# Kernel tuning notes

Measured on AMD Instinct MI355X. Metric: run time of the kernel, lower is better.

Reference implementation:

```python
import jax, jax.numpy as jnp
import numpy as np

# SpargeAttn / spas_sage2_attn_meansim block sizes
BLKQ, BLKK = 128, 64
NUM_HEADS = 8
SIMTHRESHD1 = 0.6
CDFTHRESHD = 0.98


def _block_meta(t, blk):
    # t: [B,H,S,D] -> block means [B,H,nb,D] and min-cosine-to-mean per block [B,H,nb]
    B, H, S, D = t.shape
    nb = S // blk
    tb = t.reshape(B, H, nb, blk, D)
    m = tb.mean(axis=3)
    tn = tb / (jnp.linalg.norm(tb, axis=-1, keepdims=True) + 1e-6)
    mn = m / (jnp.linalg.norm(m, axis=-1, keepdims=True) + 1e-6)
    cos = jnp.einsum('bhnkd,bhnd->bhnk', tn, mn)
    return m, cos.min(axis=-1)


def _meansim_sparse_attention(q, k, v, scale):
    # Block-sparse attention with mean-similarity pruning (SpargeAttn meansim).
    qm, qsim = _block_meta(q, BLKQ)          # [B,H,nq,D], [B,H,nq]
    km, ksim = _block_meta(k, BLKK)          # [B,H,nk,D], [B,H,nk]
    q_self = qsim > SIMTHRESHD1              # self-similar Q blocks -> mean is representative
    k_self = ksim > SIMTHRESHD1
    # pooled attention map over block means
    pooled = jax.nn.softmax(jnp.einsum('bhqd,bhkd->bhqk', qm, km) * scale, axis=-1)
    # per Q-block row: keep highest-prob K blocks until cumulative mass >= cdfthreshd
    order = jnp.argsort(-pooled, axis=-1)
    sp = jnp.take_along_axis(pooled, order, axis=-1)
    csum = jnp.cumsum(sp, axis=-1)
    keep_sorted = (csum - sp) < CDFTHRESHD   # always keeps at least the top block
    inv = jnp.argsort(order, axis=-1)
    keep = jnp.take_along_axis(keep_sorted, inv, axis=-1)  # [B,H,nq,nk]
    # conservative fallback: non-self-similar Q/K blocks are never pruned
    block_mask = keep | (~q_self)[..., None] | (~k_self)[:, :, None, :]
    tok_mask = jnp.repeat(jnp.repeat(block_mask, BLKQ, axis=2), BLKK, axis=3)
    s = jnp.einsum('bhqd,bhkd->bhqk', q, k) * scale
    s = jnp.where(tok_mask, s, -jnp.inf)
    p = jax.nn.softmax(s, axis=-1)
    return jnp.einsum('bhqk,bhkd->bhqd', p, v)


def setup_inputs() -> dict:
    key = jax.random.key(0)
    B, L, C = 2, 2048, 512
    ks = jax.random.split(key, 3)
    x = jax.random.normal(ks[0], (B, L, C), jnp.float32)
    Wqkv = jax.random.normal(ks[1], (C, 3 * C), jnp.float32) * (C ** -0.5)
    bqkv = jnp.zeros((3 * C,), jnp.float32)
    Wproj = jax.random.normal(ks[2], (C, C), jnp.float32) * (C ** -0.5)
    bproj = jnp.zeros((C,), jnp.float32)
    return {"x": x, "Wqkv": Wqkv, "bqkv": bqkv, "Wproj": Wproj, "bproj": bproj}


def reference(x, Wqkv, bqkv, Wproj, bproj):
    B, L, C = x.shape
    H = NUM_HEADS
    D = C // H
    scale = D ** -0.5
    qkv = (x @ Wqkv + bqkv).reshape(B, L, 3, H, D)
    qkv = jnp.transpose(qkv, (2, 0, 3, 1, 4))  # [3,B,H,L,D]
    q, k, v = qkv[0], qkv[1], qkv[2]
    o = _meansim_sparse_attention(q, k, v, scale)  # [B,H,L,D]
    o = jnp.transpose(o, (0, 2, 1, 3)).reshape(B, L, C)
    return o @ Wproj + bproj
```

## Files before the change

### kernel.cpp

```cpp
#include <hip/hip_runtime.h>
#include <math.h>

typedef unsigned short ushortT;
typedef unsigned int uintT;
typedef __attribute__((ext_vector_type(8))) short short8;
typedef __attribute__((ext_vector_type(16))) float f32x16;
#define MFMA32(a, b, c) __builtin_amdgcn_mfma_f32_32x32x16_bf16((a), (b), (c), 0, 0, 0)


#define LOG2E 1.4426950408889634f

static __device__ __forceinline__ ushortT f2b(float f) {
    union { float f; uintT u; } v; v.f = f;
    uintT u = v.u;
    u += 0x7fffu + ((u >> 16) & 1u);
    return (ushortT)(u >> 16);
}
static __device__ __forceinline__ uintT pack2(float a, float b) {
    return (uintT)f2b(a) | ((uintT)f2b(b) << 16);
}
static __device__ __forceinline__ uintT pack2t(float a, float b) {
    union { float f; uintT u; } x0, x1; x0.f = a; x1.f = b;
    return __builtin_amdgcn_perm(x1.u, x0.u, 0x07060302u);
}
static __device__ __forceinline__ float blo(uintT u) {
    union { uintT u; float f; } v; v.u = u << 16; return v.f;
}
static __device__ __forceinline__ float bhi(uintT u) {
    union { uintT u; float f; } v; v.u = u & 0xffff0000u; return v.f;
}
static __device__ __forceinline__ f32x16 zero16() {
    f32x16 z;
    #pragma unroll
    for (int i = 0; i < 16; ++i) z[i] = 0.f;
    return z;
}

#define NQB 16
#define NKB 32

__global__ __launch_bounds__(256) void prep_kernel(
    const float* __restrict__ x, ushortT* __restrict__ xb,
    const float* __restrict__ Wq, ushortT* __restrict__ Wqt,
    const float* __restrict__ Wp, ushortT* __restrict__ Wpt) {
    const int bid = blockIdx.x, t = threadIdx.x;
    __shared__ float tile[32][33];
    if (bid < 2048) {
        int i = (bid * 256 + t) * 4;
        float4 v = *(const float4*)(x + i);
        uint2 o; o.x = pack2(v.x, v.y); o.y = pack2(v.z, v.w);
        *(uint2*)(xb + i) = o;
        return;
    }
    const float* W; ushortT* Wt; int C, c0, r0;
    if (bid < 2816) {
        const int b = bid - 2048;
        W = Wq; Wt = Wqt; C = 1536;
        c0 = (b % 48) * 32; r0 = (b / 48) * 32;
    } else {
        const int b = bid - 2816;
        W = Wp; Wt = Wpt; C = 512;
        c0 = (b & 15) * 32; r0 = (b >> 4) * 32;
    }
    const int tx = t & 31, ty = t >> 5;
    #pragma unroll
    for (int i = 0; i < 4; ++i)
        tile[ty + 8 * i][tx] = W[(size_t)(r0 + ty + 8 * i) * C + c0 + tx];
    __syncthreads();
    #pragma unroll
    for (int i = 0; i < 4; ++i) {
        int rr = ty + 8 * i;
        Wt[(size_t)(c0 + rr) * 512 + r0 + tx] = f2b(tile[tx][rr]);
    }
}

__global__ __launch_bounds__(256) void qkv_gemm_kernel(
    const ushortT* __restrict__ xb, const ushortT* __restrict__ wt,
    const float* __restrict__ bias,
    ushortT* __restrict__ qb, ushortT* __restrict__ kbuf, ushortT* __restrict__ vt,
    float* __restrict__ qm, float* __restrict__ km,
    float* __restrict__ qs, float* __restrict__ ks) {
    __shared__ __align__(16) ushortT As[2][128 * 40];
    __shared__ __align__(16) ushortT Bs[2][64 * 40];
    __shared__ float sumbuf[4][64];
    __shared__ float meanS[2][64];
    __shared__ float wminS[4];
    const int t = threadIdx.x;
    const int l = t & 63, w = t >> 6;
    const int lm = l & 31, lh = l >> 5;
    const int rowbase = blockIdx.y * 128;
    const int colbase = blockIdx.x * 64;

    f32x16 acc[2];
    acc[0] = zero16(); acc[1] = zero16();

    const int r = t >> 1, half = t & 1;
    const ushortT* Ag = xb + (size_t)(rowbase + r) * 512 + half * 16;
    const int soA = r * 40 + half * 16;
    const int rb = t >> 2, q4 = t & 3;
    const ushortT* Bg = wt + (size_t)(colbase + rb) * 512 + q4 * 8;
    const int soB = rb * 40 + q4 * 8;

    uint4 a0, a1, b0;
    a0 = *(const uint4*)(Ag); a1 = *(const uint4*)(Ag + 8);
    b0 = *(const uint4*)(Bg);
    *(uint4*)(&As[0][soA]) = a0; *(uint4*)(&As[0][soA] + 8) = a1;
    *(uint4*)(&Bs[0][soB]) = b0;

    for (int k0 = 0; k0 < 512; k0 += 32) {
        const int cur = (k0 >> 5) & 1;
        __syncthreads();
        if (k0 < 480) {
            a0 = *(const uint4*)(Ag + k0 + 32); a1 = *(const uint4*)(Ag + k0 + 40);
            b0 = *(const uint4*)(Bg + k0 + 32);
        }
        #pragma unroll
        for (int ks2 = 0; ks2 < 2; ++ks2) {
            const int ko = 16 * ks2 + 8 * lh;
            short8 af  = *(const short8*)(&As[cur][(32 * w + lm) * 40 + ko]);
            short8 b_0 = *(const short8*)(&Bs[cur][lm * 40 + ko]);
            short8 b_1 = *(const short8*)(&Bs[cur][(32 + lm) * 40 + ko]);
            acc[0] = MFMA32(af, b_0, acc[0]);
            acc[1] = MFMA32(af, b_1, acc[1]);
        }
        if (k0 < 480) {
            const int nxt = cur ^ 1;
            *(uint4*)(&As[nxt][soA]) = a0; *(uint4*)(&As[nxt][soA] + 8) = a1;
            *(uint4*)(&Bs[nxt][soB]) = b0;
        }
    }

    const int which = blockIdx.x >> 3;
    const int h = blockIdx.x & 7;
    const int by = blockIdx.y;
    const int b = by >> 4;
    const size_t hb = (size_t)(b * 8 + h);
    float bias2[2];
    #pragma unroll
    for (int nt = 0; nt < 2; ++nt) bias2[nt] = bias[colbase + 32 * nt + lm];
    float msum[2] = {0.f, 0.f};
    #pragma unroll
    for (int nt = 0; nt < 2; ++nt) {
        const int dd = 32 * nt + lm;
        #pragma unroll
        for (int rg = 0; rg < 16; ++rg) {
            const int row_local = 32 * w + (rg & 3) + 8 * (rg >> 2) + 4 * lh;
            const int ll = (rowbase + row_local) & 2047;
            float val = acc[nt][rg] + bias2[nt];
            if (which == 0) {
                val *= 0.125f;
                msum[nt] += val;
                qb[(hb * 2048 + ll) * 64 + dd] = f2b(val * LOG2E);
            } else if (which == 1) {
                msum[nt] += val;
                kbuf[(hb * 2048 + ll) * 64 + dd] = f2b(val);
            } else {
                vt[hb * 131072 + (size_t)(ll >> 6) * 4096 + dd * 64 + (ll & 63)] = f2b(val);
            }
            acc[nt][rg] = val;
        }
    }
    if (which == 2) return;
    #pragma unroll
    for (int nt = 0; nt < 2; ++nt) {
        float s = msum[nt] + __shfl_xor(msum[nt], 32);
        if (l < 32) sumbuf[w][32 * nt + lm] = s;
    }
    __syncthreads();
    if (which == 0) {
        if (t < 64) {
            const int qbi = by & 15;
            const float m =
                (sumbuf[0][t] + sumbuf[1][t] + sumbuf[2][t] + sumbuf[3][t]) * (1.0f / 128.0f);
            qm[(hb * 16 + qbi) * 64 + t] = m;
            meanS[0][t] = m;
        }
    } else {
        if (t < 128) {
            const int d = t & 63, pair = t >> 6;
            const int kbi = 2 * (by & 15) + pair;
            const float m =
                (sumbuf[2 * pair][d] + sumbuf[2 * pair + 1][d]) * (1.0f / 64.0f);
            km[(hb * 32 + kbi) * 64 + d] = m;
            meanS[pair][d] = m;
        }
    }
    __syncthreads();
    {
        const int mrow = (which == 0) ? 0 : (w >> 1);
        const float mv0 = meanS[mrow][lm], mv1 = meanS[mrow][32 + lm];
        float mn2 = mv0 * mv0 + mv1 * mv1;
        #pragma unroll
        for (int off = 1; off < 32; off <<= 1) mn2 += __shfl_xor(mn2, off);
        const float mnorm = sqrtf(mn2);
        float cmin = 1e30f;
        #pragma unroll
        for (int rg = 0; rg < 16; ++rg) {
            float dp = acc[0][rg] * mv0 + acc[1][rg] * mv1;
            float nn = acc[0][rg] * acc[0][rg] + acc[1][rg] * acc[1][rg];
            #pragma unroll
            for (int off = 1; off < 32; off <<= 1) {
                dp += __shfl_xor(dp, off);
                nn += __shfl_xor(nn, off);
            }
            const float cosv = dp / ((sqrtf(nn) + 1e-6f) * (mnorm + 1e-6f));
            cmin = fminf(cmin, cosv);
        }
        cmin = fminf(cmin, __shfl_xor(cmin, 32));
        if (l == 0) wminS[w] = cmin;
    }
    __syncthreads();
    if (t == 0) {
        if (which == 0) {
            qs[hb * 16 + (by & 15)] =
                fminf(fminf(wminS[0], wminS[1]), fminf(wminS[2], wminS[3]));
        } else {
            ks[hb * 32 + 2 * (by & 15)]     = fminf(wminS[0], wminS[1]);
            ks[hb * 32 + 2 * (by & 15) + 1] = fminf(wminS[2], wminS[3]);
        }
    }
}

#define KS_SH (128 * 72)
#define VS_SH (64 * 136)
__global__ __launch_bounds__(512, 2) void attn_kernel(
    const ushortT* __restrict__ qb, const ushortT* __restrict__ kbuf,
    const ushortT* __restrict__ vt,
    const float* __restrict__ qm, const float* __restrict__ km,
    const float* __restrict__ qs, const float* __restrict__ ks,
    ushortT* __restrict__ ob) {
    __shared__ __align__(16) ushortT smem[2 * KS_SH + 2 * VS_SH];
    __shared__ int klist[33];
    __shared__ float qmS[64];
    __shared__ float pnS[32];
    ushortT (*Ks)[KS_SH] = (ushortT(*)[KS_SH])smem;
    ushortT (*Vs)[VS_SH] = (ushortT(*)[VS_SH])(smem + 2 * KS_SH);

    const int t = threadIdx.x;
    const int l = t & 63, w = t >> 6;
    const int lm = l & 31, lh = l >> 5;
    const int qc = w >> 2, kq = w & 3;
    const int bh = blockIdx.x, qt = blockIdx.y;

    if (t < 64) qmS[t] = qm[((size_t)bh * 16 + qt) * 64 + t];

    const ushortT* qg = qb + ((size_t)bh * 2048 + qt * 128) * 64;
    short8 qf[4][2];
    #pragma unroll
    for (int qh = 0; qh < 2; ++qh)
        #pragma unroll
        for (int ksd = 0; ksd < 4; ++ksd)
            qf[ksd][qh] = *(const short8*)(qg + (64 * qc + 32 * qh + lm) * 64 + 16 * ksd + 8 * lh);
    __syncthreads();

    if (w == 0 && l < 32) {
        const float* kmr = km + ((size_t)bh * 32 + l) * 64;
        float dot = 0.f;
        #pragma unroll
        for (int d = 0; d < 64; ++d) dot += qmS[d] * kmr[d];
        float mx = dot;
        #pragma unroll
        for (int off = 1; off < 32; off <<= 1) mx = fmaxf(mx, __shfl_xor(mx, off));
        const float e = expf(dot - mx);
        float sum = e;
        #pragma unroll
        for (int off = 1; off < 32; off <<= 1) sum += __shfl_xor(sum, off);
        const float pn = e * (1.0f / sum);
        pnS[l] = pn;
        float before = 0.f;
        #pragma unroll
        for (int j = 0; j < 32; ++j) {
            const float pj = pnS[j];
            if (pj > pn || (pj == pn && j < l)) before += pj;
        }
        const bool qfb = !(qs[bh * 16 + qt] > 0.6f);
        const bool kfb = !(ks[bh * 32 + l] > 0.6f);
        const bool keep = (before < 0.98f) || qfb || kfb;
        unsigned long long bal = __ballot(keep);
        if (keep) {
            const int rank = __popcll(bal & ((1ULL << l) - 1ULL));
            klist[rank] = l;
        }
        if (l == 0) klist[32] = __popcll(bal);
    }
    __syncthreads();

    const int cnt = klist[32];
    const int nIter = (cnt + 1) >> 1;

    const int tile = t >> 7, tt = t & 127;
    const int isV = tile >> 1, skh = tile & 1;
    const int srow = tt >> 1, shalf = (tt & 1) * 32;
    const ushortT* gsrc = (isV ? vt : kbuf) + (size_t)bh * 131072;
    const int goff = srow * 64 + shalf;
    const int soff = isV ? (srow * 136 + skh * 64 + shalf)
                         : ((skh * 64 + srow) * 72 + shalf);
    ushortT* sd0 = (isV ? &Vs[0][soff] : &Ks[0][soff]);
    ushortT* sd1 = (isV ? &Vs[1][soff] : &Ks[1][soff]);

    f32x16 oacc[2][2];
    oacc[0][0] = zero16(); oacc[1][0] = zero16();
    oacc[0][1] = zero16(); oacc[1][1] = zero16();
    float l_i[2] = {0.f, 0.f};

    uint4 st0, st1, st2, st3;
    {
        int kidx = skh; if (kidx >= cnt) kidx = cnt - 1;
        const ushortT* g = gsrc + (size_t)klist[kidx] * 4096 + goff;
        st0 = *(const uint4*)(g);      st1 = *(const uint4*)(g + 8);
        st2 = *(const uint4*)(g + 16); st3 = *(const uint4*)(g + 24);
        *(uint4*)(sd0)      = st0; *(uint4*)(sd0 + 8)  = st1;
        *(uint4*)(sd0 + 16) = st2; *(uint4*)(sd0 + 24) = st3;
    }

    for (int i = 0; i < nIter; ++i) {
        const int cur = i & 1;
        __syncthreads();
        if (i + 1 < nIter) {
            int kidx = 2 * (i + 1) + skh; if (kidx >= cnt) kidx = cnt - 1;
            const ushortT* g = gsrc + (size_t)klist[kidx] * 4096 + goff;
            st0 = *(const uint4*)(g);      st1 = *(const uint4*)(g + 8);
            st2 = *(const uint4*)(g + 16); st3 = *(const uint4*)(g + 24);
        }
        const float mf = (2 * i + (kq >> 1) < cnt) ? 1.f : 0.f;
        f32x16 sacc[2];
        sacc[0] = zero16(); sacc[1] = zero16();
        #pragma unroll
        for (int ksd = 0; ksd < 4; ++ksd) {
            const int ko = 16 * ksd + 8 * lh;
            short8 kf = *(const short8*)(&Ks[cur][(32 * kq + lm) * 72 + ko]);
            sacc[0] = MFMA32(kf, qf[ksd][0], sacc[0]);
            sacc[1] = MFMA32(kf, qf[ksd][1], sacc[1]);
        }
        uintT uu[2][4][2];
        #pragma unroll
        for (int qh = 0; qh < 2; ++qh) {
            float psum0 = 0.f, psum1 = 0.f;
            #pragma unroll
            for (int rp = 0; rp < 8; ++rp) {
                const float e0 = __builtin_amdgcn_exp2f(sacc[qh][2 * rp]) * mf;
                const float e1 = __builtin_amdgcn_exp2f(sacc[qh][2 * rp + 1]) * mf;
                psum0 += e0; psum1 += e1;
                uu[qh][rp >> 1][rp & 1] = pack2t(e0, e1);
            }
            float psum = psum0 + psum1;
            psum += __shfl_xor(psum, 32);
            l_i[qh] += psum;
        }
        #pragma unroll
        for (int ksk = 0; ksk < 2; ++ksk) {
            const int vko = 32 * kq + 16 * ksk + 8 * lh;
            short8 vf0 = *(const short8*)(&Vs[cur][lm * 136 + vko]);
            short8 vf1 = *(const short8*)(&Vs[cur][(32 + lm) * 136 + vko]);
            #pragma unroll
            for (int qh = 0; qh < 2; ++qh) {
                const uintT kA = lh ? uu[qh][2 * ksk + 1][0] : uu[qh][2 * ksk][0];
                const uintT kB = lh ? uu[qh][2 * ksk + 1][1] : uu[qh][2 * ksk][1];
                const uintT sA = lh ? uu[qh][2 * ksk][0] : uu[qh][2 * ksk + 1][0];
                const uintT sB = lh ? uu[qh][2 * ksk][1] : uu[qh][2 * ksk + 1][1];
                const uintT rA = (uintT)__shfl_xor((int)sA, 32);
                const uintT rB = (uintT)__shfl_xor((int)sB, 32);
                union { uintT u[4]; short8 v; } cv;
                if (lh == 0) { cv.u[0] = kA; cv.u[1] = kB; cv.u[2] = rA; cv.u[3] = rB; }
                else         { cv.u[0] = rA; cv.u[1] = rB; cv.u[2] = kA; cv.u[3] = kB; }
                oacc[0][qh] = MFMA32(vf0, cv.v, oacc[0][qh]);
                oacc[1][qh] = MFMA32(vf1, cv.v, oacc[1][qh]);
            }
        }
        if (i + 1 < nIter) {
            ushortT* sd = (cur ^ 1) ? sd1 : sd0;
            *(uint4*)(sd)      = st0; *(uint4*)(sd + 8)  = st1;
            *(uint4*)(sd + 16) = st2; *(uint4*)(sd + 24) = st3;
        }
    }

    uint4* ox = (uint4*)smem;
    float* lx = (float*)((char*)smem + 49152);
    __syncthreads();
    if (kq != 0) {
        const int wslot = qc * 3 + (kq - 1);
        #pragma unroll
        for (int dt = 0; dt < 2; ++dt)
            #pragma unroll
            for (int qh = 0; qh < 2; ++qh)
                #pragma unroll
                for (int g2 = 0; g2 < 2; ++g2) {
                    uint4 u;
                    u.x = pack2(oacc[dt][qh][8 * g2 + 0], oacc[dt][qh][8 * g2 + 1]);
                    u.y = pack2(oacc[dt][qh][8 * g2 + 2], oacc[dt][qh][8 * g2 + 3]);
                    u.z = pack2(oacc[dt][qh][8 * g2 + 4], oacc[dt][qh][8 * g2 + 5]);
                    u.w = pack2(oacc[dt][qh][8 * g2 + 6], oacc[dt][qh][8 * g2 + 7]);
                    ox[(wslot * 8 + (dt * 4 + qh * 2 + g2)) * 64 + l] = u;
                }
        if (lh == 0) {
            lx[(wslot * 2 + 0) * 32 + lm] = l_i[0];
            lx[(wslot * 2 + 1) * 32 + lm] = l_i[1];
        }
    }
    __syncthreads();
    if (kq == 0) {
        float lt[2] = {l_i[0], l_i[1]};
        #pragma unroll
        for (int p = 0; p < 3; ++p) {
            const int ws2 = qc * 3 + p;
            lt[0] += lx[(ws2 * 2 + 0) * 32 + lm];
            lt[1] += lx[(ws2 * 2 + 1) * 32 + lm];
            #pragma unroll
            for (int dt = 0; dt < 2; ++dt)
                #pragma unroll
                for (int qh = 0; qh < 2; ++qh)
                    #pragma unroll
                    for (int g2 = 0; g2 < 2; ++g2) {
                        uint4 u = ox[(ws2 * 8 + (dt * 4 + qh * 2 + g2)) * 64 + l];
                        oacc[dt][qh][8 * g2 + 0] += blo(u.x);
                        oacc[dt][qh][8 * g2 + 1] += bhi(u.x);
                        oacc[dt][qh][8 * g2 + 2] += blo(u.y);
                        oacc[dt][qh][8 * g2 + 3] += bhi(u.y);
                        oacc[dt][qh][8 * g2 + 4] += blo(u.z);
                        oacc[dt][qh][8 * g2 + 5] += bhi(u.z);
                        oacc[dt][qh][8 * g2 + 6] += blo(u.w);
                        oacc[dt][qh][8 * g2 + 7] += bhi(u.w);
                    }
        }
        #pragma unroll
        for (int qh = 0; qh < 2; ++qh) {
            const float inv = 1.0f / lt[qh];
            const int token = qt * 128 + qc * 64 + 32 * qh + lm;
            ushortT* orow = ob + ((size_t)bh * 2048 + token) * 64;
            #pragma unroll
            for (int dt = 0; dt < 2; ++dt)
                #pragma unroll
                for (int rp = 0; rp < 8; ++rp) {
                    const int d0 = 32 * dt + 8 * (rp >> 1) + 4 * lh + 2 * (rp & 1);
                    *(uintT*)(orow + d0) =
                        pack2(oacc[dt][qh][2 * rp] * inv, oacc[dt][qh][2 * rp + 1] * inv);
                }
        }
    }
}

__global__ __launch_bounds__(256) void proj_gemm_kernel(
    const ushortT* __restrict__ ob, const ushortT* __restrict__ wpt,
    const float* __restrict__ bias, float* __restrict__ out) {
    __shared__ __align__(16) ushortT As[2][64 * 40];
    __shared__ __align__(16) ushortT Bs[2][64 * 40];
    const int t = threadIdx.x;
    const int l = t & 63, w = t >> 6;
    const int lm = l & 31, lh = l >> 5;
    const int rh = w & 1, ch = w >> 1;
    const int rowbase = blockIdx.y * 64;
    const int colbase = blockIdx.x * 64;

    f32x16 acc = zero16();

    const int r = t >> 2, q4 = t & 3;
    const int token = rowbase + r;
    const int b2 = token >> 11, lt = token & 2047;
    const int so = r * 40 + q4 * 8;
    const ushortT* obbase = ob + ((size_t)(b2 * 8) * 2048 + lt) * 64 + q4 * 8;
    const ushortT* Bg = wpt + (size_t)(colbase + r) * 512 + q4 * 8;

    uint4 a0, b0;
    a0 = *(const uint4*)(obbase);
    b0 = *(const uint4*)(Bg);
    *(uint4*)(&As[0][so]) = a0;
    *(uint4*)(&Bs[0][so]) = b0;

    for (int k0 = 0; k0 < 512; k0 += 32) {
        const int cur = (k0 >> 5) & 1;
        __syncthreads();
        if (k0 < 480) {
            const int kn = k0 + 32;
            const ushortT* Ag = obbase + (size_t)(kn >> 6) * 131072 + (kn & 63);
            a0 = *(const uint4*)(Ag);
            b0 = *(const uint4*)(Bg + kn);
        }
        #pragma unroll
        for (int ks2 = 0; ks2 < 2; ++ks2) {
            const int ko = 16 * ks2 + 8 * lh;
            short8 af = *(const short8*)(&As[cur][(32 * rh + lm) * 40 + ko]);
            short8 bf = *(const short8*)(&Bs[cur][(32 * ch + lm) * 40 + ko]);
            acc = MFMA32(af, bf, acc);
        }
        if (k0 < 480) {
            const int nxt = cur ^ 1;
            *(uint4*)(&As[nxt][so]) = a0;
            *(uint4*)(&Bs[nxt][so]) = b0;
        }
    }
    const int c = colbase + 32 * ch + lm;
    const float bb = bias[c];
    #pragma unroll
    for (int rg = 0; rg < 16; ++rg) {
        const int row_local = 32 * rh + (rg & 3) + 8 * (rg >> 2) + 4 * lh;
        out[(size_t)(rowbase + row_local) * 512 + c] = acc[rg] + bb;
    }
}

extern "C" void kernel_launch(void* const* d_in, const int* in_sizes, int n_in,
                              void* d_out, int out_size, void* d_ws, size_t ws_size,
                              hipStream_t stream) {
    const float* x     = (const float*)d_in[0];
    const float* Wqkv  = (const float*)d_in[1];
    const float* bqkv  = (const float*)d_in[2];
    const float* Wproj = (const float*)d_in[3];
    const float* bproj = (const float*)d_in[4];
    float* out = (float*)d_out;

    char* w = (char*)d_ws;
    ushortT* xb     = (ushortT*)(w);
    ushortT* wqkvt  = (ushortT*)(w + 4194304);
    ushortT* wprojt = (ushortT*)(w + 5767168);
    ushortT* qb     = (ushortT*)(w + 6291456);
    ushortT* kbuf   = (ushortT*)(w + 10485760);
    ushortT* vt     = (ushortT*)(w + 14680064);
    ushortT* ob     = (ushortT*)(w + 18874368);
    float*   qm     = (float*)(w + 23068672);
    float*   km     = (float*)(w + 23134208);
    float*   qs     = (float*)(w + 36406272);
    float*   ks     = (float*)(w + 36407296);

    prep_kernel<<<3072, 256, 0, stream>>>(x, xb, Wqkv, wqkvt, Wproj, wprojt);
    qkv_gemm_kernel<<<dim3(24, 32), 256, 0, stream>>>(xb, wqkvt, bqkv, qb, kbuf, vt,
                                                      qm, km, qs, ks);
    attn_kernel<<<dim3(16, 16), 512, 0, stream>>>(qb, kbuf, vt, qm, km, qs, ks, ob);
    proj_gemm_kernel<<<dim3(8, 64), 256, 0, stream>>>(ob, wprojt, bproj, out);
}
```

Baseline: 134.6 us.

## Store K/V in MFMA fragment layout and load directly from global, dropping LDS staging

The QKV GEMM epilogue now writes K and V in a pre-swizzled per-lane MFMA fragment layout. The attention kernel loads its operands straight from global memory with one contiguous 16-byte load per lane, instead of double-buffering K/V tiles through shared memory with block-wide barriers. Each wave now strides over the kept K blocks independently (j += 4) rather than working in lockstep pairs, which removes the per-iteration syncthreads and the masking factor. The cost is that global-load latency is no longer hidden by explicit prefetch, and the same K/V data is fetched redundantly by the waves sharing a key block, relying on L2/L1 hits.

Result: faster. 127.3 us (-5.4%).

```diff
diff --git a/kernel.cpp b/kernel.cpp
--- a/kernel.cpp
+++ b/kernel.cpp
@@ -77,7 +77,7 @@
 __global__ __launch_bounds__(256) void qkv_gemm_kernel(
     const ushortT* __restrict__ xb, const ushortT* __restrict__ wt,
     const float* __restrict__ bias,
-    ushortT* __restrict__ qb, ushortT* __restrict__ kbuf, ushortT* __restrict__ vt,
+    ushortT* __restrict__ qb, ushortT* __restrict__ kfrag, ushortT* __restrict__ vfrag,
     float* __restrict__ qm, float* __restrict__ km,
     float* __restrict__ qs, float* __restrict__ ks) {
     __shared__ __align__(16) ushortT As[2][128 * 40];
@@ -153,9 +153,13 @@
                 qb[(hb * 2048 + ll) * 64 + dd] = f2b(val * LOG2E);
             } else if (which == 1) {
                 msum[nt] += val;
-                kbuf[(hb * 2048 + ll) * 64 + dd] = f2b(val);
+                const int koff = (((ll >> 6) * 8 + ((ll >> 5) & 1) * 4 + (dd >> 4)) << 9)
+                               + (((ll & 31) + 32 * ((dd >> 3) & 1)) << 3) + (dd & 7);
+                kfrag[hb * 131072 + koff] = f2b(val);
             } else {
-                vt[hb * 131072 + (size_t)(ll >> 6) * 4096 + dd * 64 + (ll & 63)] = f2b(val);
+                const int voff = (((ll >> 6) * 8 + (dd >> 5) * 4 + ((ll >> 4) & 3)) << 9)
+                               + (((dd & 31) + 32 * ((ll >> 3) & 1)) << 3) + (ll & 7);
+                vfrag[hb * 131072 + voff] = f2b(val);
             }
             acc[nt][rg] = val;
         }
@@ -221,20 +225,17 @@
     }
 }
 
-#define KS_SH (128 * 72)
-#define VS_SH (64 * 136)
 __global__ __launch_bounds__(512, 2) void attn_kernel(
-    const ushortT* __restrict__ qb, const ushortT* __restrict__ kbuf,
-    const ushortT* __restrict__ vt,
+    const ushortT* __restrict__ qb, const ushortT* __restrict__ kfrag,
+    const ushortT* __restrict__ vfrag,
     const float* __restrict__ qm, const float* __restrict__ km,
     const float* __restrict__ qs, const float* __restrict__ ks,
     ushortT* __restrict__ ob) {
-    __shared__ __align__(16) ushortT smem[2 * KS_SH + 2 * VS_SH];
+    __shared__ __align__(16) uint4 ox[6 * 8 * 64];
+    __shared__ float lx[6 * 2 * 32];
     __shared__ int klist[33];
     __shared__ float qmS[64];
     __shared__ float pnS[32];
-    ushortT (*Ks)[KS_SH] = (ushortT(*)[KS_SH])smem;
-    ushortT (*Vs)[VS_SH] = (ushortT(*)[VS_SH])(smem + 2 * KS_SH);
 
     const int t = threadIdx.x;
     const int l = t & 63, w = t >> 6;
@@ -286,97 +287,66 @@
     __syncthreads();
 
     const int cnt = klist[32];
-    const int nIter = (cnt + 1) >> 1;
-
-    const int tile = t >> 7, tt = t & 127;
-    const int isV = tile >> 1, skh = tile & 1;
-    const int srow = tt >> 1, shalf = (tt & 1) * 32;
-    const ushortT* gsrc = (isV ? vt : kbuf) + (size_t)bh * 131072;
-    const int goff = srow * 64 + shalf;
-    const int soff = isV ? (srow * 136 + skh * 64 + shalf)
-                         : ((skh * 64 + srow) * 72 + shalf);
-    ushortT* sd0 = (isV ? &Vs[0][soff] : &Ks[0][soff]);
-    ushortT* sd1 = (isV ? &Vs[1][soff] : &Ks[1][soff]);
+    const ushortT* kfb = kfrag + (size_t)bh * 131072;
+    const ushortT* vfb = vfrag + (size_t)bh * 131072;
 
     f32x16 oacc[2][2];
     oacc[0][0] = zero16(); oacc[1][0] = zero16();
     oacc[0][1] = zero16(); oacc[1][1] = zero16();
     float l_i[2] = {0.f, 0.f};
 
-    uint4 st0, st1, st2, st3;
-    {
-        int kidx = skh; if (kidx >= cnt) kidx = cnt - 1;
-        const ushortT* g = gsrc + (size_t)klist[kidx] * 4096 + goff;
-        st0 = *(const uint4*)(g);      st1 = *(const uint4*)(g + 8);
-        st2 = *(const uint4*)(g + 16); st3 = *(const uint4*)(g + 24);
-        *(uint4*)(sd0)      = st0; *(uint4*)(sd0 + 8)  = st1;
-        *(uint4*)(sd0 + 16) = st2; *(uint4*)(sd0 + 24) = st3;
-    }
-
-    for (int i = 0; i < nIter; ++i) {
-        const int cur = i & 1;
-        __syncthreads();
-        if (i + 1 < nIter) {
-            int kidx = 2 * (i + 1) + skh; if (kidx >= cnt) kidx = cnt - 1;
-            const ushortT* g = gsrc + (size_t)klist[kidx] * 4096 + goff;
-            st0 = *(const uint4*)(g);      st1 = *(const uint4*)(g + 8);
-            st2 = *(const uint4*)(g + 16); st3 = *(const uint4*)(g + 24);
-        }
-        const float mf = (2 * i + (kq >> 1) < cnt) ? 1.f : 0.f;
-        f32x16 sacc[2];
-        sacc[0] = zero16(); sacc[1] = zero16();
-        #pragma unroll
-        for (int ksd = 0; ksd < 4; ++ksd) {
-            const int ko = 16 * ksd + 8 * lh;
-            short8 kf = *(const short8*)(&Ks[cur][(32 * kq + lm) * 72 + ko]);
-            sacc[0] = MFMA32(kf, qf[ksd][0], sacc[0]);
-            sacc[1] = MFMA32(kf, qf[ksd][1], sacc[1]);
-        }
-        uintT uu[2][4][2];
-        #pragma unroll
-        for (int qh = 0; qh < 2; ++qh) {
-            float psum0 = 0.f, psum1 = 0.f;
-            #pragma unroll
-            for (int rp = 0; rp < 8; ++rp) {
-                const float e0 = __builtin_amdgcn_exp2f(sacc[qh][2 * rp]) * mf;
-                const float e1 = __builtin_amdgcn_exp2f(sacc[qh][2 * rp + 1]) * mf;
-                psum0 += e0; psum1 += e1;
-                uu[qh][rp >> 1][rp & 1] = pack2t(e0, e1);
+    for (int j = kq; j < cnt; j += 4) {
+        const int kb = klist[j];
+        const ushortT* kbase = kfb + kb * 4096;
+        const ushortT* vbase = vfb + kb * 4096;
+        #pragma unroll
+        for (int kh = 0; kh < 2; ++kh) {
+            f32x16 sacc[2];
+            sacc[0] = zero16(); sacc[1] = zero16();
+            #pragma unroll
+            for (int ksd = 0; ksd < 4; ++ksd) {
+                short8 kf = *(const short8*)(kbase + ((kh * 4 + ksd) << 9) + l * 8);
+                sacc[0] = MFMA32(kf, qf[ksd][0], sacc[0]);
+                sacc[1] = MFMA32(kf, qf[ksd][1], sacc[1]);
             }
-            float psum = psum0 + psum1;
-            psum += __shfl_xor(psum, 32);
-            l_i[qh] += psum;
-        }
-        #pragma unroll
-        for (int ksk = 0; ksk < 2; ++ksk) {
-            const int vko = 32 * kq + 16 * ksk + 8 * lh;
-            short8 vf0 = *(const short8*)(&Vs[cur][lm * 136 + vko]);
-            short8 vf1 = *(const short8*)(&Vs[cur][(32 + lm) * 136 + vko]);
+            uintT uu[2][4][2];
             #pragma unroll
             for (int qh = 0; qh < 2; ++qh) {
-                const uintT kA = lh ? uu[qh][2 * ksk + 1][0] : uu[qh][2 * ksk][0];
-                const uintT kB = lh ? uu[qh][2 * ksk + 1][1] : uu[qh][2 * ksk][1];
-                const uintT sA = lh ? uu[qh][2 * ksk][0] : uu[qh][2 * ksk + 1][0];
-                const uintT sB = lh ? uu[qh][2 * ksk][1] : uu[qh][2 * ksk + 1][1];
-                const uintT rA = (uintT)__shfl_xor((int)sA, 32);
-                const uintT rB = (uintT)__shfl_xor((int)sB, 32);
-                union { uintT u[4]; short8 v; } cv;
-                if (lh == 0) { cv.u[0] = kA; cv.u[1] = kB; cv.u[2] = rA; cv.u[3] = rB; }
-                else         { cv.u[0] = rA; cv.u[1] = rB; cv.u[2] = kA; cv.u[3] = kB; }
-                oacc[0][qh] = MFMA32(vf0, cv.v, oacc[0][qh]);
-                oacc[1][qh] = MFMA32(vf1, cv.v, oacc[1][qh]);
+                float psum0 = 0.f, psum1 = 0.f;
+                #pragma unroll
+                for (int rp = 0; rp < 8; ++rp) {
+                    const float e0 = __builtin_amdgcn_exp2f(sacc[qh][2 * rp]);
+                    const float e1 = __builtin_amdgcn_exp2f(sacc[qh][2 * rp + 1]);
+                    psum0 += e0; psum1 += e1;
+                    uu[qh][rp >> 1][rp & 1] = pack2t(e0, e1);
+                }
+                float psum = psum0 + psum1;
+                psum += __shfl_xor(psum, 32);
+                l_i[qh] += psum;
             }
-        }
-        if (i + 1 < nIter) {
-            ushortT* sd = (cur ^ 1) ? sd1 : sd0;
-            *(uint4*)(sd)      = st0; *(uint4*)(sd + 8)  = st1;
-            *(uint4*)(sd + 16) = st2; *(uint4*)(sd + 24) = st3;
-        }
-    }
-
-    uint4* ox = (uint4*)smem;
-    float* lx = (float*)((char*)smem + 49152);
-    __syncthreads();
+            #pragma unroll
+            for (int ksk = 0; ksk < 2; ++ksk) {
+                const int ksl = 2 * kh + ksk;
+                short8 vf0 = *(const short8*)(vbase + (ksl << 9) + l * 8);
+                short8 vf1 = *(const short8*)(vbase + ((4 + ksl) << 9) + l * 8);
+                #pragma unroll
+                for (int qh = 0; qh < 2; ++qh) {
+                    const uintT kA = lh ? uu[qh][2 * ksk + 1][0] : uu[qh][2 * ksk][0];
+                    const uintT kB = lh ? uu[qh][2 * ksk + 1][1] : uu[qh][2 * ksk][1];
+                    const uintT sA = lh ? uu[qh][2 * ksk][0] : uu[qh][2 * ksk + 1][0];
+                    const uintT sB = lh ? uu[qh][2 * ksk][1] : uu[qh][2 * ksk + 1][1];
+                    const uintT rA = (uintT)__shfl_xor((int)sA, 32);
+                    const uintT rB = (uintT)__shfl_xor((int)sB, 32);
+                    union { uintT u[4]; short8 v; } cv;
+                    if (lh == 0) { cv.u[0] = kA; cv.u[1] = kB; cv.u[2] = rA; cv.u[3] = rB; }
+                    else         { cv.u[0] = rA; cv.u[1] = rB; cv.u[2] = kA; cv.u[3] = kB; }
+                    oacc[0][qh] = MFMA32(vf0, cv.v, oacc[0][qh]);
+                    oacc[1][qh] = MFMA32(vf1, cv.v, oacc[1][qh]);
+                }
+            }
+        }
+    }
+
     if (kq != 0) {
         const int wslot = qc * 3 + (kq - 1);
         #pragma unroll
@@ -512,8 +482,8 @@
     ushortT* wqkvt  = (ushortT*)(w + 4194304);
     ushortT* wprojt = (ushortT*)(w + 5767168);
     ushortT* qb     = (ushortT*)(w + 6291456);
-    ushortT* kbuf   = (ushortT*)(w + 10485760);
-    ushortT* vt     = (ushortT*)(w + 14680064);
+    ushortT* kfrag  = (ushortT*)(w + 10485760);
+    ushortT* vfrag  = (ushortT*)(w + 14680064);
     ushortT* ob     = (ushortT*)(w + 18874368);
     float*   qm     = (float*)(w + 23068672);
     float*   km     = (float*)(w + 23134208);
@@ -521,8 +491,8 @@
     float*   ks     = (float*)(w + 36407296);
 
     prep_kernel<<<3072, 256, 0, stream>>>(x, xb, Wqkv, wqkvt, Wproj, wprojt);
-    qkv_gemm_kernel<<<dim3(24, 32), 256, 0, stream>>>(xb, wqkvt, bqkv, qb, kbuf, vt,
+    qkv_gemm_kernel<<<dim3(24, 32), 256, 0, stream>>>(xb, wqkvt, bqkv, qb, kfrag, vfrag,
                                                       qm, km, qs, ks);
-    attn_kernel<<<dim3(16, 16), 512, 0, stream>>>(qb, kbuf, vt, qm, km, qs, ks, ob);
+    attn_kernel<<<dim3(16, 16), 512, 0, stream>>>(qb, kfrag, vfrag, qm, km, qs, ks, ob);
     proj_gemm_kernel<<<dim3(8, 64), 256, 0, stream>>>(ob, wprojt, bproj, out);
 }
```
